# Performance work log

Hardware: AMD Instinct MI355X
Metric: run time of the kernel (lower is better)

Reference implementation:

```python
import jax, jax.numpy as jnp
import numpy as np

C = 256
CQK = C // 8  # query/key projection dim (in_dim // 8)
B, H, W = 4, 64, 64


def setup_inputs() -> dict:
    key = jax.random.key(0)
    ks = jax.random.split(key, 7)
    scale = 0.05
    x = jax.random.normal(ks[0], (B, C, H, W), dtype=jnp.float32)
    Wq = jax.random.normal(ks[1], (CQK, C), dtype=jnp.float32) * scale
    bq = jax.random.normal(ks[2], (CQK,), dtype=jnp.float32) * scale
    Wk = jax.random.normal(ks[3], (CQK, C), dtype=jnp.float32) * scale
    bk = jax.random.normal(ks[4], (CQK,), dtype=jnp.float32) * scale
    Wv = jax.random.normal(ks[5], (C, C), dtype=jnp.float32) * scale
    bv = jax.random.normal(ks[6], (C,), dtype=jnp.float32) * scale
    return {"x": x, "Wq": Wq, "bq": bq, "Wk": Wk, "bk": bk, "Wv": Wv, "bv": bv}


def reference(x, Wq, bq, Wk, bk, Wv, bv):
    b, c, h, w = x.shape
    n = h * w
    xf = x.reshape(b, c, n)  # [B, C, N]
    # 1x1 convs == per-pixel linear maps over channels
    q = jnp.einsum('dc,bcn->bnd', Wq, xf) + bq[None, None, :]   # [B, N, C/8]
    k = jnp.einsum('dc,bcn->bdn', Wk, xf) + bk[None, :, None]   # [B, C/8, N]
    v = jnp.einsum('dc,bcn->bdn', Wv, xf) + bv[None, :, None]   # [B, C, N]
    energy = jnp.einsum('bnd,bdm->bnm', q, k)                    # [B, N, N]
    attention = jax.nn.softmax(energy, axis=-1)                  # softmax over keys
    # out = V @ attention^T  (torch: bmm(proj_value, attention.permute(0,2,1)))
    out = jnp.einsum('bdm,bnm->bdn', v, attention)               # [B, C, N]
    return out.reshape(b, c, h, w) + x
```

## Files before the change

### kernel.cpp

```cpp
#include <hip/hip_runtime.h>
#include <math.h>

#define BATCH 4
#define CH    256
#define NPIX  4096
#define DQK   32

typedef short          s16;
typedef unsigned int   uint_t;
typedef __attribute__((ext_vector_type(8))) short short8;
typedef __attribute__((ext_vector_type(4))) float floatx4;
typedef __attribute__((ext_vector_type(16))) float floatx16;

__device__ __forceinline__ s16 f2bf(float f) {
  union { float f; uint_t u; } v; v.f = f;
  return (s16)((v.u + 0x8000u) >> 16);
}
__device__ __forceinline__ uint_t pk2(float a, float b) {
  union { float f; uint_t u; } x, y; x.f = a; y.f = b;
  return (((y.u + 0x8000u) >> 16) << 16) | ((x.u + 0x8000u) >> 16);
}
__device__ __forceinline__ float fexp2(float x) {
#if defined(__has_builtin)
#if __has_builtin(__builtin_amdgcn_exp2f)
  return __builtin_amdgcn_exp2f(x);
#else
  float r; asm("v_exp_f32 %0, %1" : "=v"(r) : "v"(x)); return r;
#endif
#else
  float r; asm("v_exp_f32 %0, %1" : "=v"(r) : "v"(x)); return r;
#endif
}

__global__ __launch_bounds__(256) void prepack(
    const float* __restrict__ Wq, const float* __restrict__ bq,
    const float* __restrict__ Wk, const float* __restrict__ bk,
    const float* __restrict__ Wv, const float* __restrict__ bv,
    s16* __restrict__ Wbf, float* __restrict__ Bsw)
{
  const float LOG2E = 1.4426950408889634f;
  const int gid = blockIdx.x * 256 + threadIdx.x;
  const int e0  = gid * 4;
  const int row = e0 >> 8, col = e0 & 255;
  const float* src = (row < 32) ? Wq + (size_t)row * 256
                   : (row < 64) ? Wk + (size_t)(row - 32) * 256
                                : Wv + (size_t)(row - 64) * 256;
  float4 f = *(const float4*)(src + col);
  const float sc = (row < 32) ? LOG2E : 1.f;
  uint2 o; o.x = pk2(f.x * sc, f.y * sc); o.y = pk2(f.z * sc, f.w * sc);
  *(uint2*)(Wbf + e0) = o;
  if (gid < 320)
    Bsw[gid] = (gid < 32) ? bq[gid] * LOG2E
             : (gid < 64) ? bk[gid - 32] : bv[gid - 64];
}

__global__ __launch_bounds__(256, 2) void proj_mfma(
    const float* __restrict__ x, const s16* __restrict__ Wbf,
    const float* __restrict__ Bsw,
    s16* __restrict__ Qw, s16* __restrict__ Kw, s16* __restrict__ Vw)
{
  const int b  = blockIdx.x >> 7;
  const int n0 = (blockIdx.x & 127) << 5;
  const int t  = threadIdx.x;

  __shared__ s16 Xs[32][264];
  __shared__ s16 Os[256][40];

  const float* xb = x + (size_t)b * CH * NPIX + n0;
  #pragma unroll
  for (int i = 0; i < 2; ++i) {
    int task = i * 256 + t;
    int ncg  = task & 7;
    int kcg  = task >> 3;
    const float* src = xb + (size_t)(kcg * 4) * NPIX + ncg * 4;
    float rows[4][4];
    *(float4*)&rows[0][0] = *(const float4*)(src);
    *(float4*)&rows[1][0] = *(const float4*)(src + NPIX);
    *(float4*)&rows[2][0] = *(const float4*)(src + 2 * NPIX);
    *(float4*)&rows[3][0] = *(const float4*)(src + 3 * NPIX);
    #pragma unroll
    for (int c = 0; c < 4; ++c) {
      uint2 pk;
      pk.x = pk2(rows[0][c], rows[1][c]);
      pk.y = pk2(rows[2][c], rows[3][c]);
      *(uint2*)&Xs[ncg * 4 + c][kcg * 4] = pk;
    }
  }
  __syncthreads();

  const int w    = t >> 6;
  const int l15  = t & 15;
  const int quad = (t & 63) >> 4;

  floatx4 acc[5][2];
  #pragma unroll
  for (int si = 0; si < 5; ++si)
    #pragma unroll
    for (int nt = 0; nt < 2; ++nt) acc[si][nt] = (floatx4){0.f, 0.f, 0.f, 0.f};

  short8 afc[5], afn[5];
  #pragma unroll
  for (int si = 0; si < 5; ++si) {
    const int s = w + si * 4;
    afc[si] = *(const short8*)(Wbf + (size_t)(s * 16 + l15) * 256 + quad * 8);
  }
  for (int kc = 0; kc < 8; ++kc) {
    const int k0  = kc * 32;
    const int kn0 = (kc < 7) ? k0 + 32 : 0;
    #pragma unroll
    for (int si = 0; si < 5; ++si) {
      const int s = w + si * 4;
      afn[si] = *(const short8*)(Wbf + (size_t)(s * 16 + l15) * 256 + kn0 + quad * 8);
    }
    short8 bf[2];
    #pragma unroll
    for (int nt = 0; nt < 2; ++nt)
      bf[nt] = *(const short8*)&Xs[l15 + 16 * nt][k0 + quad * 8];
    #pragma unroll
    for (int si = 0; si < 5; ++si)
      #pragma unroll
      for (int nt = 0; nt < 2; ++nt)
        acc[si][nt] = __builtin_amdgcn_mfma_f32_16x16x32_bf16(afc[si], bf[nt], acc[si][nt], 0, 0, 0);
    #pragma unroll
    for (int si = 0; si < 5; ++si) afc[si] = afn[si];
  }

  #pragma unroll
  for (int si = 0; si < 5; ++si) {
    const int s = w + si * 4;
    float4 bb = *(const float4*)(Bsw + 16 * s + quad * 4);
    #pragma unroll
    for (int nt = 0; nt < 2; ++nt) {
      const int px  = 16 * nt + l15;
      float v0 = acc[si][nt][0] + bb.x;
      float v1 = acc[si][nt][1] + bb.y;
      float v2 = acc[si][nt][2] + bb.z;
      float v3 = acc[si][nt][3] + bb.w;
      if (s < 4) {
        s16* dst = (s < 2) ? Qw : Kw;
        int d0 = (s & 1) * 16 + quad * 4;
        uint2 pq; pq.x = pk2(v0, v1); pq.y = pk2(v2, v3);
        *(uint2*)(dst + ((size_t)b * NPIX + n0 + px) * DQK + d0) = pq;
      } else {
        const int c0 = (s - 4) * 16 + quad * 4;
        Os[c0 + 0][px] = f2bf(v0);
        Os[c0 + 1][px] = f2bf(v1);
        Os[c0 + 2][px] = f2bf(v2);
        Os[c0 + 3][px] = f2bf(v3);
      }
    }
  }
  __syncthreads();
  #pragma unroll
  for (int rep = 0; rep < 4; ++rep) {
    const int task = rep * 256 + t;
    const int fid  = task >> 6;
    const int ln   = task & 63;
    const int c    = fid >> 1;
    const int sl   = fid & 1;
    const int row  = c * 32 + (ln & 31);
    const int col  = sl * 16 + (ln >> 5) * 8;
    *(uint4*)(Vw + (((size_t)b * 8 + c) * 256 + (n0 >> 4) + sl) * 512 + ln * 8) =
        *(const uint4*)&Os[row][col];
  }
}

__global__ __launch_bounds__(1024, 4) void attn_mfma(
    const s16* __restrict__ Qw, const s16* __restrict__ Kw,
    const s16* __restrict__ Vt, const float* __restrict__ x,
    float* __restrict__ out)
{
  const int bi = blockIdx.x;
  const int b  = bi & 3;
  const int qt = bi >> 2;
  const int n0 = qt * 64;
  const int t  = threadIdx.x;
  const int w    = t >> 6;
  const int lane = t & 63;
  const int l15  = t & 15;
  const int quad = lane >> 4;
  const int l31  = t & 31;
  const int lh   = lane >> 5;
  const int l7   = t & 7;
  const int sw   = w & 7;
  const int sq   = w >> 3;
  const int kh   = sq;

  __shared__ s16  Pt[2][64][128];
  __shared__ float Lsum[64][8];
  __shared__ float Ored[8][32][64];

  const s16* qbase = Qw + ((size_t)b * NPIX + n0 + sq * 32) * DQK;
  short8 qb[2];
  #pragma unroll
  for (int tq = 0; tq < 2; ++tq)
    qb[tq] = *(const short8*)(qbase + (size_t)(16 * tq + l15) * DQK + quad * 8);

  floatx16 o[2];
  #pragma unroll
  for (int i = 0; i < 16; ++i) { o[0][i] = 0.f; o[1][i] = 0.f; }
  float l_part[2] = {0.f, 0.f};

  const s16* kbase = Kw + (size_t)b * NPIX * DQK;
  const s16* vtb   = Vt + ((size_t)(b * 8 + sw) * 256) * 512 + lane * 8;

  short8 ka_c, ka_n, va[4];
  ka_c = *(const short8*)(kbase + (size_t)(16 * sw + l15) * DQK + quad * 8);
  #pragma unroll
  for (int ks = 0; ks < 4; ++ks)
    va[ks] = *(const short8*)(vtb + (size_t)(ks + 4 * kh) * 512);

  const int wslot = (((2 * sw + (quad >> 1)) ^ l7) << 3) + (quad & 1) * 4;

  {
    floatx4 sacc[2];
    #pragma unroll
    for (int tq = 0; tq < 2; ++tq)
      sacc[tq] = __builtin_amdgcn_mfma_f32_16x16x32_bf16(
                   ka_c, qb[tq], (floatx4){0.f, 0.f, 0.f, 0.f}, 0, 0, 0);
    ka_n = *(const short8*)(kbase + (size_t)(128 + 16 * sw + l15) * DQK + quad * 8);
    #pragma unroll
    for (int tq = 0; tq < 2; ++tq) {
      float p0 = fexp2(fminf(sacc[tq][0], 86.f));
      float p1 = fexp2(fminf(sacc[tq][1], 86.f));
      float p2 = fexp2(fminf(sacc[tq][2], 86.f));
      float p3 = fexp2(fminf(sacc[tq][3], 86.f));
      l_part[tq] += (p0 + p1) + (p2 + p3);
      uint2 pk; pk.x = pk2(p0, p1); pk.y = pk2(p2, p3);
      *(uint2*)&Pt[0][sq * 32 + 16 * tq + l15][wslot] = pk;
    }
    ka_c = ka_n;
  }
  __syncthreads();

  for (int kt = 0; kt < 32; ++kt) {
    const int buf = kt & 1;

    short8 pb[4][2];
    #pragma unroll
    for (int ks = 0; ks < 4; ++ks) {
      const int rslot = ((2 * (ks + 4 * kh) + lh) ^ l7) << 3;
      pb[ks][0] = *(const short8*)&Pt[buf][l31     ][rslot];
      pb[ks][1] = *(const short8*)&Pt[buf][32 + l31][rslot];
    }

    if (kt < 31) {
      floatx4 sacc[2];
      #pragma unroll
      for (int tq = 0; tq < 2; ++tq)
        sacc[tq] = __builtin_amdgcn_mfma_f32_16x16x32_bf16(
                     ka_c, qb[tq], (floatx4){0.f, 0.f, 0.f, 0.f}, 0, 0, 0);
      const int mn2 = (kt < 30) ? (kt + 2) * 128 : 0;
      ka_n = *(const short8*)(kbase + (size_t)(mn2 + 16 * sw + l15) * DQK + quad * 8);
      #pragma unroll
      for (int tq = 0; tq < 2; ++tq) {
        float p0 = fexp2(fminf(sacc[tq][0], 86.f));
        float p1 = fexp2(fminf(sacc[tq][1], 86.f));
        float p2 = fexp2(fminf(sacc[tq][2], 86.f));
        float p3 = fexp2(fminf(sacc[tq][3], 86.f));
        l_part[tq] += (p0 + p1) + (p2 + p3);
        uint2 pk; pk.x = pk2(p0, p1); pk.y = pk2(p2, p3);
        *(uint2*)&Pt[buf ^ 1][sq * 32 + 16 * tq + l15][wslot] = pk;
      }
      ka_c = ka_n;
    }

    __builtin_amdgcn_s_setprio(1);
    #pragma unroll
    for (int ks = 0; ks < 4; ++ks) {
      o[0] = __builtin_amdgcn_mfma_f32_32x32x16_bf16(va[ks], pb[ks][0], o[0], 0, 0, 0);
      o[1] = __builtin_amdgcn_mfma_f32_32x32x16_bf16(va[ks], pb[ks][1], o[1], 0, 0, 0);
    }
    __builtin_amdgcn_s_setprio(0);

    const int sn = ((kt + 1) & 31) * 8;
    #pragma unroll
    for (int ks = 0; ks < 4; ++ks)
      va[ks] = *(const short8*)(vtb + (size_t)(sn + ks + 4 * kh) * 512);

    __syncthreads();
  }

  #pragma unroll
  for (int tq = 0; tq < 2; ++tq) {
    l_part[tq] += __shfl_xor(l_part[tq], 16);
    l_part[tq] += __shfl_xor(l_part[tq], 32);
  }
  if (quad == 0) {
    #pragma unroll
    for (int tq = 0; tq < 2; ++tq) Lsum[sq * 32 + 16 * tq + l15][sw] = l_part[tq];
  }
  if (kh == 1) {
    #pragma unroll
    for (int r = 0; r < 16; ++r) {
      const int chrow = (r & 3) + 8 * (r >> 2) + 4 * lh;
      Ored[sw][chrow][l31]      = o[0][r];
      Ored[sw][chrow][32 + l31] = o[1][r];
    }
  }
  __syncthreads();

  if (kh == 0) {
    const int q0 = l31, q1 = 32 + l31;
    float4 a0 = *(const float4*)&Lsum[q0][0];
    float4 a1 = *(const float4*)&Lsum[q0][4];
    float4 b0 = *(const float4*)&Lsum[q1][0];
    float4 b1 = *(const float4*)&Lsum[q1][4];
    float inv0 = 1.f / (((a0.x + a0.y) + (a0.z + a0.w)) +
                        ((a1.x + a1.y) + (a1.z + a1.w)));
    float inv1 = 1.f / (((b0.x + b0.y) + (b0.z + b0.w)) +
                        ((b1.x + b1.y) + (b1.z + b1.w)));
    #pragma unroll
    for (int r = 0; r < 16; ++r) {
      const int chrow = (r & 3) + 8 * (r >> 2) + 4 * lh;
      const int ch = sw * 32 + chrow;
      const float s0 = o[0][r] + Ored[sw][chrow][l31];
      const float s1 = o[1][r] + Ored[sw][chrow][32 + l31];
      const size_t off0 = ((size_t)b * CH + ch) * NPIX + n0 + q0;
      const size_t off1 = ((size_t)b * CH + ch) * NPIX + n0 + q1;
      out[off0] = fmaf(s0, inv0, x[off0]);
      out[off1] = fmaf(s1, inv1, x[off1]);
    }
  }
}

extern "C" void kernel_launch(void* const* d_in, const int* in_sizes, int n_in,
                              void* d_out, int out_size, void* d_ws, size_t ws_size,
                              hipStream_t stream) {
  (void)in_sizes; (void)n_in; (void)out_size; (void)ws_size;
  const float* x  = (const float*)d_in[0];
  const float* Wq = (const float*)d_in[1];
  const float* bq = (const float*)d_in[2];
  const float* Wk = (const float*)d_in[3];
  const float* bk = (const float*)d_in[4];
  const float* Wv = (const float*)d_in[5];
  const float* bv = (const float*)d_in[6];
  float* out = (float*)d_out;

  unsigned char* ws = (unsigned char*)d_ws;
  s16*   Qw  = (s16*)ws;
  s16*   Kw  = (s16*)(ws + (size_t)1 * 1024 * 1024);
  s16*   Vt  = (s16*)(ws + (size_t)2 * 1024 * 1024);
  s16*   Wbf = (s16*)(ws + (size_t)10 * 1024 * 1024);
  float* Bsw = (float*)(ws + (size_t)10 * 1024 * 1024 + 256 * 1024);

  hipLaunchKernelGGL(prepack, dim3(80), dim3(256), 0, stream,
                     Wq, bq, Wk, bk, Wv, bv, Wbf, Bsw);
  hipLaunchKernelGGL(proj_mfma, dim3(512), dim3(256), 0, stream,
                     x, Wbf, Bsw, Qw, Kw, Vt);
  hipLaunchKernelGGL(attn_mfma, dim3(256), dim3(1024), 0, stream,
                     Qw, Kw, Vt, x, out);
}
```

Before: 137.0 us.

## Double key tile per iteration and software-pipeline P reads with MFMAs

Each iteration now processes 256 keys instead of 128. Every wave computes scores for all 64 queries against its own 16-key slice, and the two key-halves split the PV accumulation over 8 k-steps each. This halves the number of loop iterations and __syncthreads barriers. It also interleaves LDS reads of the P tile with the PV MFMAs via a two-register ping-pong, and aliases Ored onto the Pt shared buffer so the larger P tile fits. In exchange each thread holds more registers (8 V fragments, 4 Q fragments, 4 score accumulators), which may pressure occupancy under the 1024-thread launch bound, and shared memory per block grows.

```diff
diff --git a/kernel.cpp b/kernel.cpp
--- a/kernel.cpp
+++ b/kernel.cpp
@@ -182,120 +182,127 @@
   const int l31  = t & 31;
   const int lh   = lane >> 5;
   const int l7   = t & 7;
-  const int sw   = w & 7;
-  const int sq   = w >> 3;
-  const int kh   = sq;
-
-  __shared__ s16  Pt[2][64][128];
-  __shared__ float Lsum[64][8];
-  __shared__ float Ored[8][32][64];
-
-  const s16* qbase = Qw + ((size_t)b * NPIX + n0 + sq * 32) * DQK;
-  short8 qb[2];
-  #pragma unroll
-  for (int tq = 0; tq < 2; ++tq)
+  const int cpv  = w & 7;
+  const int kh   = w >> 3;
+
+  __shared__ __align__(16) unsigned char smem[69632];
+  s16   (*Pt)[64][256]   = reinterpret_cast<s16 (*)[64][256]>(smem);
+  float (*Ored)[32][64]  = reinterpret_cast<float (*)[32][64]>(smem);
+  float (*Lsum)[16]      = reinterpret_cast<float (*)[16]>(smem + 65536);
+
+  const s16* qbase = Qw + ((size_t)b * NPIX + n0) * DQK;
+  short8 qb[4];
+  #pragma unroll
+  for (int tq = 0; tq < 4; ++tq)
     qb[tq] = *(const short8*)(qbase + (size_t)(16 * tq + l15) * DQK + quad * 8);
 
   floatx16 o[2];
   #pragma unroll
   for (int i = 0; i < 16; ++i) { o[0][i] = 0.f; o[1][i] = 0.f; }
-  float l_part[2] = {0.f, 0.f};
+  float l_part[4] = {0.f, 0.f, 0.f, 0.f};
 
   const s16* kbase = Kw + (size_t)b * NPIX * DQK;
-  const s16* vtb   = Vt + ((size_t)(b * 8 + sw) * 256) * 512 + lane * 8;
-
-  short8 ka_c, ka_n, va[4];
-  ka_c = *(const short8*)(kbase + (size_t)(16 * sw + l15) * DQK + quad * 8);
-  #pragma unroll
-  for (int ks = 0; ks < 4; ++ks)
-    va[ks] = *(const short8*)(vtb + (size_t)(ks + 4 * kh) * 512);
-
-  const int wslot = (((2 * sw + (quad >> 1)) ^ l7) << 3) + (quad & 1) * 4;
+  const s16* vtb   = Vt + ((size_t)(b * 8 + cpv) * 256) * 512 + lane * 8;
+
+  short8 ka_c, ka_n, va[8];
+  ka_c = *(const short8*)(kbase + (size_t)(16 * w + l15) * DQK + quad * 8);
+  #pragma unroll
+  for (int ks = 0; ks < 8; ++ks)
+    va[ks] = *(const short8*)(vtb + (size_t)(ks + 8 * kh) * 512);
+
+  const int wslot = (((2 * w + (quad >> 1)) ^ l7) << 3) + (quad & 1) * 4;
 
   {
-    floatx4 sacc[2];
-    #pragma unroll
-    for (int tq = 0; tq < 2; ++tq)
+    floatx4 sacc[4];
+    #pragma unroll
+    for (int tq = 0; tq < 4; ++tq)
       sacc[tq] = __builtin_amdgcn_mfma_f32_16x16x32_bf16(
                    ka_c, qb[tq], (floatx4){0.f, 0.f, 0.f, 0.f}, 0, 0, 0);
-    ka_n = *(const short8*)(kbase + (size_t)(128 + 16 * sw + l15) * DQK + quad * 8);
-    #pragma unroll
-    for (int tq = 0; tq < 2; ++tq) {
+    ka_n = *(const short8*)(kbase + (size_t)(256 + 16 * w + l15) * DQK + quad * 8);
+    #pragma unroll
+    for (int tq = 0; tq < 4; ++tq) {
       float p0 = fexp2(fminf(sacc[tq][0], 86.f));
       float p1 = fexp2(fminf(sacc[tq][1], 86.f));
       float p2 = fexp2(fminf(sacc[tq][2], 86.f));
       float p3 = fexp2(fminf(sacc[tq][3], 86.f));
       l_part[tq] += (p0 + p1) + (p2 + p3);
       uint2 pk; pk.x = pk2(p0, p1); pk.y = pk2(p2, p3);
-      *(uint2*)&Pt[0][sq * 32 + 16 * tq + l15][wslot] = pk;
+      *(uint2*)&Pt[0][16 * tq + l15][wslot] = pk;
     }
     ka_c = ka_n;
   }
   __syncthreads();
 
-  for (int kt = 0; kt < 32; ++kt) {
-    const int buf = kt & 1;
-
-    short8 pb[4][2];
-    #pragma unroll
-    for (int ks = 0; ks < 4; ++ks) {
-      const int rslot = ((2 * (ks + 4 * kh) + lh) ^ l7) << 3;
-      pb[ks][0] = *(const short8*)&Pt[buf][l31     ][rslot];
-      pb[ks][1] = *(const short8*)&Pt[buf][32 + l31][rslot];
-    }
-
-    if (kt < 31) {
-      floatx4 sacc[2];
+#define PB_RD(P, KSL, KG) {                                                  \
+    const int rs = ((2 * (8 * kh + (KG)) + lh) ^ l7) << 3;                   \
+    pc##P[KSL][0] = *(const short8*)&Pt[buf][l31     ][rs];                  \
+    pc##P[KSL][1] = *(const short8*)&Pt[buf][32 + l31][rs]; }
+#define PB_MM(P, KSL, KG) {                                                  \
+    o[0] = __builtin_amdgcn_mfma_f32_32x32x16_bf16(va[KG], pc##P[KSL][0], o[0], 0, 0, 0); \
+    o[1] = __builtin_amdgcn_mfma_f32_32x32x16_bf16(va[KG], pc##P[KSL][1], o[1], 0, 0, 0); }
+
+  for (int kt2 = 0; kt2 < 16; ++kt2) {
+    const int buf = kt2 & 1;
+    short8 pc0[2][2], pc1[2][2];
+
+    PB_RD(0, 0, 0); PB_RD(0, 1, 1);
+
+    if (kt2 < 15) {
+      floatx4 sacc[4];
       #pragma unroll
-      for (int tq = 0; tq < 2; ++tq)
+      for (int tq = 0; tq < 4; ++tq)
         sacc[tq] = __builtin_amdgcn_mfma_f32_16x16x32_bf16(
                      ka_c, qb[tq], (floatx4){0.f, 0.f, 0.f, 0.f}, 0, 0, 0);
-      const int mn2 = (kt < 30) ? (kt + 2) * 128 : 0;
-      ka_n = *(const short8*)(kbase + (size_t)(mn2 + 16 * sw + l15) * DQK + quad * 8);
+      const int mn2 = (kt2 < 14) ? (kt2 + 2) * 256 : 0;
+      ka_n = *(const short8*)(kbase + (size_t)(mn2 + 16 * w + l15) * DQK + quad * 8);
       #pragma unroll
-      for (int tq = 0; tq < 2; ++tq) {
+      for (int tq = 0; tq < 4; ++tq) {
         float p0 = fexp2(fminf(sacc[tq][0], 86.f));
         float p1 = fexp2(fminf(sacc[tq][1], 86.f));
         float p2 = fexp2(fminf(sacc[tq][2], 86.f));
         float p3 = fexp2(fminf(sacc[tq][3], 86.f));
         l_part[tq] += (p0 + p1) + (p2 + p3);
         uint2 pk; pk.x = pk2(p0, p1); pk.y = pk2(p2, p3);
-        *(uint2*)&Pt[buf ^ 1][sq * 32 + 16 * tq + l15][wslot] = pk;
+        *(uint2*)&Pt[buf ^ 1][16 * tq + l15][wslot] = pk;
       }
       ka_c = ka_n;
     }
 
     __builtin_amdgcn_s_setprio(1);
-    #pragma unroll
-    for (int ks = 0; ks < 4; ++ks) {
-      o[0] = __builtin_amdgcn_mfma_f32_32x32x16_bf16(va[ks], pb[ks][0], o[0], 0, 0, 0);
-      o[1] = __builtin_amdgcn_mfma_f32_32x32x16_bf16(va[ks], pb[ks][1], o[1], 0, 0, 0);
-    }
+    PB_RD(1, 0, 2); PB_RD(1, 1, 3);
+    PB_MM(0, 0, 0); PB_MM(0, 1, 1);
+    PB_RD(0, 0, 4); PB_RD(0, 1, 5);
+    PB_MM(1, 0, 2); PB_MM(1, 1, 3);
+    PB_RD(1, 0, 6); PB_RD(1, 1, 7);
+    PB_MM(0, 0, 4); PB_MM(0, 1, 5);
+    PB_MM(1, 0, 6); PB_MM(1, 1, 7);
     __builtin_amdgcn_s_setprio(0);
 
-    const int sn = ((kt + 1) & 31) * 8;
-    #pragma unroll
-    for (int ks = 0; ks < 4; ++ks)
-      va[ks] = *(const short8*)(vtb + (size_t)(sn + ks + 4 * kh) * 512);
+    const int sn = ((kt2 + 1) & 15) * 16;
+    #pragma unroll
+    for (int ks = 0; ks < 8; ++ks)
+      va[ks] = *(const short8*)(vtb + (size_t)(sn + 8 * kh + ks) * 512);
 
     __syncthreads();
   }
-
-  #pragma unroll
-  for (int tq = 0; tq < 2; ++tq) {
+#undef PB_RD
+#undef PB_MM
+
+  #pragma unroll
+  for (int tq = 0; tq < 4; ++tq) {
     l_part[tq] += __shfl_xor(l_part[tq], 16);
     l_part[tq] += __shfl_xor(l_part[tq], 32);
   }
   if (quad == 0) {
     #pragma unroll
-    for (int tq = 0; tq < 2; ++tq) Lsum[sq * 32 + 16 * tq + l15][sw] = l_part[tq];
+    for (int tq = 0; tq < 4; ++tq) Lsum[16 * tq + l15][w] = l_part[tq];
   }
   if (kh == 1) {
     #pragma unroll
     for (int r = 0; r < 16; ++r) {
       const int chrow = (r & 3) + 8 * (r >> 2) + 4 * lh;
-      Ored[sw][chrow][l31]      = o[0][r];
-      Ored[sw][chrow][32 + l31] = o[1][r];
+      Ored[cpv][chrow][l31]      = o[0][r];
+      Ored[cpv][chrow][32 + l31] = o[1][r];
     }
   }
   __syncthreads();
@@ -304,18 +311,26 @@
     const int q0 = l31, q1 = 32 + l31;
     float4 a0 = *(const float4*)&Lsum[q0][0];
     float4 a1 = *(const float4*)&Lsum[q0][4];
+    float4 a2 = *(const float4*)&Lsum[q0][8];
+    float4 a3 = *(const float4*)&Lsum[q0][12];
     float4 b0 = *(const float4*)&Lsum[q1][0];
     float4 b1 = *(const float4*)&Lsum[q1][4];
-    float inv0 = 1.f / (((a0.x + a0.y) + (a0.z + a0.w)) +
-                        ((a1.x + a1.y) + (a1.z + a1.w)));
-    float inv1 = 1.f / (((b0.x + b0.y) + (b0.z + b0.w)) +
-                        ((b1.x + b1.y) + (b1.z + b1.w)));
+    float4 b2 = *(const float4*)&Lsum[q1][8];
+    float4 b3 = *(const float4*)&Lsum[q1][12];
+    float inv0 = 1.f / ((((a0.x + a0.y) + (a0.z + a0.w)) +
+                         ((a1.x + a1.y) + (a1.z + a1.w))) +
+                        (((a2.x + a2.y) + (a2.z + a2.w)) +
+                         ((a3.x + a3.y) + (a3.z + a3.w))));
+    float inv1 = 1.f / ((((b0.x + b0.y) + (b0.z + b0.w)) +
+                         ((b1.x + b1.y) + (b1.z + b1.w))) +
+                        (((b2.x + b2.y) + (b2.z + b2.w)) +
+                         ((b3.x + b3.y) + (b3.z + b3.w))));
     #pragma unroll
     for (int r = 0; r < 16; ++r) {
       const int chrow = (r & 3) + 8 * (r >> 2) + 4 * lh;
-      const int ch = sw * 32 + chrow;
-      const float s0 = o[0][r] + Ored[sw][chrow][l31];
-      const float s1 = o[1][r] + Ored[sw][chrow][32 + l31];
+      const int ch = cpv * 32 + chrow;
+      const float s0 = o[0][r] + Ored[cpv][chrow][l31];
+      const float s1 = o[1][r] + Ored[cpv][chrow][32 + l31];
       const size_t off0 = ((size_t)b * CH + ch) * NPIX + n0 + q0;
       const size_t off1 = ((size_t)b * CH + ch) * NPIX + n0 + q1;
       out[off0] = fmaf(s0, inv0, x[off0]);
```

Measured after the change: 176.5 us. 28.8% more time.

## Shrink attention query tile to 32 and drop split-K output reduction

Applied to the files above, without the earlier changes.

Changes the attention kernel from 64-query tiles with 16 waves (two key halves reduced through shared memory) to 32-query tiles with 8 waves, each wave owning 32 channels over the full key range, and doubles the grid to 512 blocks. This removes the Ored shared-memory reduction and its extra synchronisation and halves per-block LDS. In exchange, each K tile and its softmax exponentials now serve only 32 queries, so QK^T work, exp work and K/V global traffic per query double.

```diff
diff --git a/kernel.cpp b/kernel.cpp
--- a/kernel.cpp
+++ b/kernel.cpp
@@ -165,7 +165,7 @@
   }
 }
 
-__global__ __launch_bounds__(1024, 4) void attn_mfma(
+__global__ __launch_bounds__(512, 4) void attn_mfma(
     const s16* __restrict__ Qw, const s16* __restrict__ Kw,
     const s16* __restrict__ Vt, const float* __restrict__ x,
     float* __restrict__ out)
@@ -173,7 +173,7 @@
   const int bi = blockIdx.x;
   const int b  = bi & 3;
   const int qt = bi >> 2;
-  const int n0 = qt * 64;
+  const int n0 = qt * 32;
   const int t  = threadIdx.x;
   const int w    = t >> 6;
   const int lane = t & 63;
@@ -182,35 +182,31 @@
   const int l31  = t & 31;
   const int lh   = lane >> 5;
   const int l7   = t & 7;
-  const int sw   = w & 7;
-  const int sq   = w >> 3;
-  const int kh   = sq;
-
-  __shared__ s16  Pt[2][64][128];
-  __shared__ float Lsum[64][8];
-  __shared__ float Ored[8][32][64];
-
-  const s16* qbase = Qw + ((size_t)b * NPIX + n0 + sq * 32) * DQK;
+
+  __shared__ s16  Pt[2][32][128];
+  __shared__ float Lsum[32][8];
+
+  const s16* qbase = Qw + ((size_t)b * NPIX + n0) * DQK;
   short8 qb[2];
   #pragma unroll
   for (int tq = 0; tq < 2; ++tq)
     qb[tq] = *(const short8*)(qbase + (size_t)(16 * tq + l15) * DQK + quad * 8);
 
-  floatx16 o[2];
-  #pragma unroll
-  for (int i = 0; i < 16; ++i) { o[0][i] = 0.f; o[1][i] = 0.f; }
+  floatx16 o;
+  #pragma unroll
+  for (int i = 0; i < 16; ++i) o[i] = 0.f;
   float l_part[2] = {0.f, 0.f};
 
   const s16* kbase = Kw + (size_t)b * NPIX * DQK;
-  const s16* vtb   = Vt + ((size_t)(b * 8 + sw) * 256) * 512 + lane * 8;
-
-  short8 ka_c, ka_n, va[4];
-  ka_c = *(const short8*)(kbase + (size_t)(16 * sw + l15) * DQK + quad * 8);
-  #pragma unroll
-  for (int ks = 0; ks < 4; ++ks)
-    va[ks] = *(const short8*)(vtb + (size_t)(ks + 4 * kh) * 512);
-
-  const int wslot = (((2 * sw + (quad >> 1)) ^ l7) << 3) + (quad & 1) * 4;
+  const s16* vtb   = Vt + ((size_t)(b * 8 + w) * 256) * 512 + lane * 8;
+
+  short8 ka_c, ka_n, va[8];
+  ka_c = *(const short8*)(kbase + (size_t)(16 * w + l15) * DQK + quad * 8);
+  #pragma unroll
+  for (int ks = 0; ks < 8; ++ks)
+    va[ks] = *(const short8*)(vtb + (size_t)ks * 512);
+
+  const int wslot = (((2 * w + (quad >> 1)) ^ l7) << 3) + (quad & 1) * 4;
 
   {
     floatx4 sacc[2];
@@ -218,7 +214,7 @@
     for (int tq = 0; tq < 2; ++tq)
       sacc[tq] = __builtin_amdgcn_mfma_f32_16x16x32_bf16(
                    ka_c, qb[tq], (floatx4){0.f, 0.f, 0.f, 0.f}, 0, 0, 0);
-    ka_n = *(const short8*)(kbase + (size_t)(128 + 16 * sw + l15) * DQK + quad * 8);
+    ka_n = *(const short8*)(kbase + (size_t)(128 + 16 * w + l15) * DQK + quad * 8);
     #pragma unroll
     for (int tq = 0; tq < 2; ++tq) {
       float p0 = fexp2(fminf(sacc[tq][0], 86.f));
@@ -227,7 +223,7 @@
       float p3 = fexp2(fminf(sacc[tq][3], 86.f));
       l_part[tq] += (p0 + p1) + (p2 + p3);
       uint2 pk; pk.x = pk2(p0, p1); pk.y = pk2(p2, p3);
-      *(uint2*)&Pt[0][sq * 32 + 16 * tq + l15][wslot] = pk;
+      *(uint2*)&Pt[0][16 * tq + l15][wslot] = pk;
     }
     ka_c = ka_n;
   }
@@ -236,12 +232,11 @@
   for (int kt = 0; kt < 32; ++kt) {
     const int buf = kt & 1;
 
-    short8 pb[4][2];
-    #pragma unroll
-    for (int ks = 0; ks < 4; ++ks) {
-      const int rslot = ((2 * (ks + 4 * kh) + lh) ^ l7) << 3;
-      pb[ks][0] = *(const short8*)&Pt[buf][l31     ][rslot];
-      pb[ks][1] = *(const short8*)&Pt[buf][32 + l31][rslot];
+    short8 pb[8];
+    #pragma unroll
+    for (int ks = 0; ks < 8; ++ks) {
+      const int rslot = ((2 * ks + lh) ^ l7) << 3;
+      pb[ks] = *(const short8*)&Pt[buf][l31][rslot];
     }
 
     if (kt < 31) {
@@ -251,7 +246,7 @@
         sacc[tq] = __builtin_amdgcn_mfma_f32_16x16x32_bf16(
                      ka_c, qb[tq], (floatx4){0.f, 0.f, 0.f, 0.f}, 0, 0, 0);
       const int mn2 = (kt < 30) ? (kt + 2) * 128 : 0;
-      ka_n = *(const short8*)(kbase + (size_t)(mn2 + 16 * sw + l15) * DQK + quad * 8);
+      ka_n = *(const short8*)(kbase + (size_t)(mn2 + 16 * w + l15) * DQK + quad * 8);
       #pragma unroll
       for (int tq = 0; tq < 2; ++tq) {
         float p0 = fexp2(fminf(sacc[tq][0], 86.f));
@@ -260,23 +255,21 @@
         float p3 = fexp2(fminf(sacc[tq][3], 86.f));
         l_part[tq] += (p0 + p1) + (p2 + p3);
         uint2 pk; pk.x = pk2(p0, p1); pk.y = pk2(p2, p3);
-        *(uint2*)&Pt[buf ^ 1][sq * 32 + 16 * tq + l15][wslot] = pk;
+        *(uint2*)&Pt[buf ^ 1][16 * tq + l15][wslot] = pk;
       }
       ka_c = ka_n;
     }
 
     __builtin_amdgcn_s_setprio(1);
     #pragma unroll
-    for (int ks = 0; ks < 4; ++ks) {
-      o[0] = __builtin_amdgcn_mfma_f32_32x32x16_bf16(va[ks], pb[ks][0], o[0], 0, 0, 0);
-      o[1] = __builtin_amdgcn_mfma_f32_32x32x16_bf16(va[ks], pb[ks][1], o[1], 0, 0, 0);
-    }
+    for (int ks = 0; ks < 8; ++ks)
+      o = __builtin_amdgcn_mfma_f32_32x32x16_bf16(va[ks], pb[ks], o, 0, 0, 0);
     __builtin_amdgcn_s_setprio(0);
 
     const int sn = ((kt + 1) & 31) * 8;
     #pragma unroll
-    for (int ks = 0; ks < 4; ++ks)
-      va[ks] = *(const short8*)(vtb + (size_t)(sn + ks + 4 * kh) * 512);
+    for (int ks = 0; ks < 8; ++ks)
+      va[ks] = *(const short8*)(vtb + (size_t)(sn + ks) * 512);
 
     __syncthreads();
   }
@@ -288,38 +281,21 @@
   }
   if (quad == 0) {
     #pragma unroll
-    for (int tq = 0; tq < 2; ++tq) Lsum[sq * 32 + 16 * tq + l15][sw] = l_part[tq];
-  }
-  if (kh == 1) {
+    for (int tq = 0; tq < 2; ++tq) Lsum[16 * tq + l15][w] = l_part[tq];
+  }
+  __syncthreads();
+
+  {
+    const int q = l31;
+    float4 s0 = *(const float4*)&Lsum[q][0];
+    float4 s1 = *(const float4*)&Lsum[q][4];
+    float invq = 1.f / (((s0.x + s0.y) + (s0.z + s0.w)) +
+                        ((s1.x + s1.y) + (s1.z + s1.w)));
     #pragma unroll
     for (int r = 0; r < 16; ++r) {
-      const int chrow = (r & 3) + 8 * (r >> 2) + 4 * lh;
-      Ored[sw][chrow][l31]      = o[0][r];
-      Ored[sw][chrow][32 + l31] = o[1][r];
-    }
-  }
-  __syncthreads();
-
-  if (kh == 0) {
-    const int q0 = l31, q1 = 32 + l31;
-    float4 a0 = *(const float4*)&Lsum[q0][0];
-    float4 a1 = *(const float4*)&Lsum[q0][4];
-    float4 b0 = *(const float4*)&Lsum[q1][0];
-    float4 b1 = *(const float4*)&Lsum[q1][4];
-    float inv0 = 1.f / (((a0.x + a0.y) + (a0.z + a0.w)) +
-                        ((a1.x + a1.y) + (a1.z + a1.w)));
-    float inv1 = 1.f / (((b0.x + b0.y) + (b0.z + b0.w)) +
-                        ((b1.x + b1.y) + (b1.z + b1.w)));
-    #pragma unroll
-    for (int r = 0; r < 16; ++r) {
-      const int chrow = (r & 3) + 8 * (r >> 2) + 4 * lh;
-      const int ch = sw * 32 + chrow;
-      const float s0 = o[0][r] + Ored[sw][chrow][l31];
-      const float s1 = o[1][r] + Ored[sw][chrow][32 + l31];
-      const size_t off0 = ((size_t)b * CH + ch) * NPIX + n0 + q0;
-      const size_t off1 = ((size_t)b * CH + ch) * NPIX + n0 + q1;
-      out[off0] = fmaf(s0, inv0, x[off0]);
-      out[off1] = fmaf(s1, inv1, x[off1]);
+      const int ch = 32 * w + (r & 3) + 8 * (r >> 2) + 4 * lh;
+      const size_t off = ((size_t)b * CH + ch) * NPIX + n0 + q;
+      out[off] = fmaf(o[r], invq, x[off]);
     }
   }
 }
@@ -348,6 +324,6 @@
                      Wq, bq, Wk, bk, Wv, bv, Wbf, Bsw);
   hipLaunchKernelGGL(proj_mfma, dim3(512), dim3(256), 0, stream,
                      x, Wbf, Bsw, Qw, Kw, Vt);
-  hipLaunchKernelGGL(attn_mfma, dim3(256), dim3(1024), 0, stream,
+  hipLaunchKernelGGL(attn_mfma, dim3(512), dim3(512), 0, stream,
                      Qw, Kw, Vt, x, out);
 }
```

Result: slower. 142.9 us (+4.3%).
